# Kernel tuning notes

Measured on AMD Instinct MI355X. Metric: run time of the kernel, lower is better.

The kernel has to match this reference:

```python
import jax, jax.numpy as jnp
import numpy as np

DT = 0.5
T_STEPS = int(2500 / DT)   # 5000
T_STIM = int(2000 / DT)    # 4000
A = 270.0; B_ = 108.0; D_ = 0.154; GAMMA = 0.641; TAU_S = 100.0; TAU_AMPA = 2.0
BATCH = 4096


def setup_inputs() -> dict:
    key = jax.random.key(0)
    k0, k1, k2, k3, k4 = jax.random.split(key, 5)
    return {
        "input_signal": jax.random.normal(k0, (BATCH, 1), dtype=jnp.float32),
        "J11": jnp.float32(0.2609), "J12": jnp.float32(0.0497),
        "J21": jnp.float32(0.0497), "J22": jnp.float32(0.2609),
        "J_ext": jnp.float32(0.0156), "I_0": jnp.float32(0.3255),
        "noise_ampa": jnp.float32(0.02), "threshold": jnp.float32(0.5),
        "motor_delay": jnp.float32(0.1),
        "eps0_1": jax.random.normal(k1, (BATCH, 1), dtype=jnp.float32),
        "eps0_2": jax.random.normal(k2, (BATCH, 1), dtype=jnp.float32),
        "eps_1": jax.random.normal(k3, (T_STEPS, BATCH, 1), dtype=jnp.float32),
        "eps_2": jax.random.normal(k4, (T_STEPS, BATCH, 1), dtype=jnp.float32),
    }


def _H(x):
    # Wong-Wang f-I curve: relu((a x - b) / (1 - exp(-d (a x - b)) + 1e-6))
    u = A * x - B_
    return jax.nn.relu(u / (1.0 - jnp.exp(-D_ * u) + 1e-6))


def _simulate(input_signal, J11, J12, J21, J22, J_ext, I_0, noise_ampa,
              eps0_1, eps0_2, eps_1, eps_2):
    decay = jnp.exp(jnp.float32(-DT / TAU_AMPA))
    nscale = jnp.float32(np.sqrt((1.0 - np.exp(-2.0 * DT / TAU_AMPA)) / 2.0))
    s0 = jnp.full_like(input_signal, 0.1)  # [B,1]
    carry0 = (s0, s0, eps0_1 * noise_ampa, eps0_2 * noise_ampa)

    def step(carry, xs):
        s1, s2, In1, In2 = carry
        e1, e2, t = xs
        stim = t < T_STIM
        I1 = jnp.where(stim, J_ext * (1.0 + input_signal / 100.0), 0.0)
        I2 = jnp.where(stim, J_ext * (1.0 - input_signal / 100.0), 0.0)
        x1 = J11 * s1 - J12 * s2 + I_0 + I1 + In1
        x2 = J22 * s2 - J21 * s1 + I_0 + I2 + In2
        ds1 = -(s1 / TAU_S) + (1.0 - s1) * _H(x1) * GAMMA / 1000.0
        ds2 = -(s2 / TAU_S) + (1.0 - s2) * _H(x2) * GAMMA / 1000.0
        In1n = In1 * decay + noise_ampa * nscale * e1
        In2n = In2 * decay + noise_ampa * nscale * e2
        s1n = s1 + ds1 * DT
        s2n = s2 + ds2 * DT
        ys = (jnp.concatenate([s1n, s2n], axis=-1),   # trajectory row [B,2]
              jnp.concatenate([ds1, ds2], axis=-1))   # dsdt row [B,2]
        return (s1n, s2n, In1n, In2n), ys

    ts = jnp.arange(T_STEPS)
    _, (traj, dsdt) = jax.lax.scan(step, carry0, (eps_1, eps_2, ts))
    return traj, dsdt  # each [T, B, 2]


def _decide(traj_m):
    # traj_m = trajectory - threshold; first-crossing times per unit
    m1 = traj_m[:, :, 0] > 0
    m2 = traj_m[:, :, 1] > 0
    inf = jnp.float32(jnp.inf)
    t1 = jnp.where(m1.any(0), jnp.argmax(m1, axis=0).astype(jnp.float32), inf)
    t2 = jnp.where(m2.any(0), jnp.argmax(m2, axis=0).astype(jnp.float32), inf)
    dtimes = jnp.where(t1 < t2, t1, -t2)
    return dtimes * DT


def reference(input_signal, J11, J12, J21, J22, J_ext, I_0, noise_ampa,
              threshold, motor_delay, eps0_1, eps0_2, eps_1, eps_2):
    traj, dsdt = _simulate(input_signal, J11, J12, J21, J22, J_ext, I_0,
                           noise_ampa, eps0_1, eps0_2, eps_1, eps_2)
    out = _decide(traj - threshold)  # [B], signed decision time in ms
    out = jnp.where(out < 0, out / 1000.0 - motor_delay,
                    jnp.where(out > 0, out / 1000.0 + motor_delay, out))
    return out
```

## Files before the change

kernel.cpp:

```cpp
#include <hip/hip_runtime.h>

#define BATCHN 4096
#define NSTEPS 5000
#define NSTIM  4000
#define U      25
#define NBLK      (NSTEPS / U)
#define NBLK_STIM (NSTIM / U)
#define ELPB   32

static __device__ __forceinline__ float swap_pair(float v) {
    return __int_as_float(
        __builtin_amdgcn_mov_dpp(__float_as_int(v), 0xB1, 0xF, 0xF, true));
}

__global__ __launch_bounds__(128, 1) void ww_kernel(
    const float* __restrict__ input_signal,
    const float* __restrict__ sJ11, const float* __restrict__ sJ12,
    const float* __restrict__ sJ21, const float* __restrict__ sJ22,
    const float* __restrict__ sJext, const float* __restrict__ sI0,
    const float* __restrict__ sNoise, const float* __restrict__ sThr,
    const float* __restrict__ sDelay,
    const float* __restrict__ eps0_1, const float* __restrict__ eps0_2,
    const float* __restrict__ eps_1, const float* __restrict__ eps_2,
    float* __restrict__ out)
{
    __shared__ float slab[2][U][64];
    __shared__ float strc[2][U][64];
    __shared__ int done1;
    __shared__ int exit_blk;

    const int tid  = threadIdx.x;
    const int lane = tid & 63;
    const int wave = tid >> 6;
    const int unit = lane & 1;

    const float KE = -0.22217503629690245f;

    if (wave == 0) {
        __builtin_amdgcn_s_setprio(3);
        const float J11 = sJ11[0], J12 = sJ12[0], J21 = sJ21[0], J22 = sJ22[0];
        const float K270 = KE * 270.0f;
        const float B11 = K270 * J11, nB12 = -K270 * J12;
        const float B22 = K270 * J22, nB21 = -K270 * J21;
        const float Bs = unit ? B22 : B11;
        const float Bc = unit ? nB21 : nB12;
        const float nKE  = -KE;
        const float KE1p = 1.000001f * KE;
        const float SM = 0.995f;
        const float QC = 3.205e-4f;

        float s = 0.1f;

        if (lane == 0) { done1 = 0; exit_blk = 0x7fffffff; }
        __syncthreads();
        bool wrote = false;
        for (int blk = 0; blk < NBLK; ++blk) {
            if (blk >= *(volatile int*)&exit_blk) break;
            if (!wrote && *(volatile int*)&done1) {
                if (lane == 0) exit_blk = blk + 1;
                wrote = true;
            }
            const int sl = blk & 1;
            const float* __restrict__ base = &slab[sl][0][lane];
            float* __restrict__ trc = &strc[sl][0][lane];
            float k0 = base[0];
            float k1 = base[64];
            #pragma unroll
            for (int i = 0; i < U; ++i) {
                float kc = k0;
                k0 = k1;
                if (i + 2 < U) k1 = base[(i + 2) * 64];
                float sc = swap_pair(s);
                float w  = fmaf(Bs, s, fmaf(Bc, sc, kc));
                float x  = __builtin_amdgcn_exp2f(w);
                float r  = __builtin_amdgcn_rcpf(fmaf(nKE, x, KE1p));
                float h  = fmaxf(w * r, 0.0f);
                s = fmaf(h, fmaf(-QC, s, QC), SM * s);
                trc[i * 64] = s;
            }
            __syncthreads();
        }
        return;
    }

    const int b = blockIdx.x * ELPB + (lane >> 1);
    const float noise = sNoise[0];
    const float Jext = sJext[0], I0 = sI0[0];
    const float thr = sThr[0], delay = sDelay[0];

    const float inp = input_signal[b];
    const float Pself = unit
        ? fmaf(270.0f, I0 + Jext * (1.0f - inp * 0.01f), -108.0f)
        : fmaf(270.0f, I0 + Jext * (1.0f + inp * 0.01f), -108.0f);
    const float Pn  = fmaf(270.0f, I0, -108.0f);
    const float KPs = KE * Pself, KPn = KE * Pn;

    const float decay = 0.7788007830714049f;
    const float kKE   = KE * noise * 0.4435478165294536f * 270.0f;
    const float n270K = noise * 270.0f * KE;

    const float* __restrict__ ep = (unit ? eps_2 : eps_1) + b;
    float VK = (unit ? eps0_2[b] : eps0_1[b]) * n270K;

    auto fill = [&](int blk) {
        const int sl = blk & 1;
        const size_t off = (size_t)blk * U * BATCHN;
        const float KP = (blk < NBLK_STIM) ? KPs : KPn;
        float* __restrict__ dst = &slab[sl][0][lane];
        float r[U];
        #pragma unroll
        for (int i = 0; i < U; ++i)
            r[i] = ep[off + (size_t)i * BATCHN];
        #pragma unroll
        for (int i = 0; i < U; ++i) {
            dst[i * 64] = VK + KP;
            VK = fmaf(VK, decay, kKE * r[i]);
        }
    };

    const float INF = __builtin_inff();
    float tm = INF;
    float tf = 0.0f;
    bool mydone = false;

    auto scan = [&](int blk) {
        const int sl = blk & 1;
        const float* __restrict__ src = &strc[sl][0][lane];
        #pragma unroll
        for (int i = 0; i < U; ++i) {
            float sv = src[i * 64];
            tm = fminf(tm, (sv > thr) ? tf : INF);
            tf += 1.0f;
        }
    };

    fill(0);
    __syncthreads();
    for (int blk = 0; blk < NBLK; ++blk) {
        if (blk >= *(volatile int*)&exit_blk) break;
        if (blk + 1 < NBLK) fill(blk + 1);
        if (blk >= 1) {
            scan(blk - 1);
            if (!mydone) {
                float pm = fminf(tm, swap_pair(tm));
                if (__all(pm < INF)) {
                    if (lane == 0) done1 = 1;
                    mydone = true;
                }
            }
        }
        __syncthreads();
    }
    if (!mydone) scan(NBLK - 1);

    float to = swap_pair(tm);
    if (unit == 0) {
        float t1 = tm, t2 = to;
        float o;
        if (t1 == INF && t2 == INF) {
            o = -3.0e38f;
        } else {
            float dtm = (t1 < t2) ? t1 : -t2;
            o = dtm * 0.5f;
            if (o < 0.0f)      o = o / 1000.0f - delay;
            else if (o > 0.0f) o = o / 1000.0f + delay;
        }
        out[b] = o;
    }
}

extern "C" void kernel_launch(void* const* d_in, const int* in_sizes, int n_in,
                              void* d_out, int out_size, void* d_ws, size_t ws_size,
                              hipStream_t stream) {
    ww_kernel<<<dim3(BATCHN / ELPB), dim3(128), 0, stream>>>(
        (const float*)d_in[0],
        (const float*)d_in[1],
        (const float*)d_in[2],
        (const float*)d_in[3],
        (const float*)d_in[4],
        (const float*)d_in[5],
        (const float*)d_in[6],
        (const float*)d_in[7],
        (const float*)d_in[8],
        (const float*)d_in[9],
        (const float*)d_in[10],
        (const float*)d_in[11],
        (const float*)d_in[12],
        (const float*)d_in[13],
        (float*)d_out);
}
```

Measured before the change: 428.7 us.

## Merge producer and consumer waves into one wave with register double-buffered noise

Replaces the two-wave design, where a loader wave filled LDS slabs and a compute wave ran the recurrence, with a single wave per block. That wave prefetches noise into two register buffers, computes the noise recurrence inline, and checks the threshold crossing on the fly. This removes the LDS traffic, the barriers and the shared early-exit flags. The cost is that global load latency is no longer hidden by a separate wave and must be covered by software prefetch one block ahead, and register pressure goes up.

```diff
diff --git a/kernel.cpp b/kernel.cpp
--- a/kernel.cpp
+++ b/kernel.cpp
@@ -13,7 +13,7 @@
         __builtin_amdgcn_mov_dpp(__float_as_int(v), 0xB1, 0xF, 0xF, true));
 }
 
-__global__ __launch_bounds__(128, 1) void ww_kernel(
+__global__ __launch_bounds__(64, 1) void ww_kernel(
     const float* __restrict__ input_signal,
     const float* __restrict__ sJ11, const float* __restrict__ sJ12,
     const float* __restrict__ sJ21, const float* __restrict__ sJ22,
@@ -24,66 +24,23 @@
     const float* __restrict__ eps_1, const float* __restrict__ eps_2,
     float* __restrict__ out)
 {
-    __shared__ float slab[2][U][64];
-    __shared__ float strc[2][U][64];
-    __shared__ int done1;
-    __shared__ int exit_blk;
-
-    const int tid  = threadIdx.x;
-    const int lane = tid & 63;
-    const int wave = tid >> 6;
+    const int lane = threadIdx.x;
     const int unit = lane & 1;
+    const int b    = blockIdx.x * ELPB + (lane >> 1);
 
     const float KE = -0.22217503629690245f;
 
-    if (wave == 0) {
-        __builtin_amdgcn_s_setprio(3);
-        const float J11 = sJ11[0], J12 = sJ12[0], J21 = sJ21[0], J22 = sJ22[0];
-        const float K270 = KE * 270.0f;
-        const float B11 = K270 * J11, nB12 = -K270 * J12;
-        const float B22 = K270 * J22, nB21 = -K270 * J21;
-        const float Bs = unit ? B22 : B11;
-        const float Bc = unit ? nB21 : nB12;
-        const float nKE  = -KE;
-        const float KE1p = 1.000001f * KE;
-        const float SM = 0.995f;
-        const float QC = 3.205e-4f;
+    const float J11 = sJ11[0], J12 = sJ12[0], J21 = sJ21[0], J22 = sJ22[0];
+    const float K270 = KE * 270.0f;
+    const float B11 = K270 * J11, nB12 = -K270 * J12;
+    const float B22 = K270 * J22, nB21 = -K270 * J21;
+    const float Bs = unit ? B22 : B11;
+    const float Bc = unit ? nB21 : nB12;
+    const float nKE  = -KE;
+    const float KE1p = 1.000001f * KE;
+    const float SM = 0.995f;
+    const float QC = 3.205e-4f;
 
-        float s = 0.1f;
-
-        if (lane == 0) { done1 = 0; exit_blk = 0x7fffffff; }
-        __syncthreads();
-        bool wrote = false;
-        for (int blk = 0; blk < NBLK; ++blk) {
-            if (blk >= *(volatile int*)&exit_blk) break;
-            if (!wrote && *(volatile int*)&done1) {
-                if (lane == 0) exit_blk = blk + 1;
-                wrote = true;
-            }
-            const int sl = blk & 1;
-            const float* __restrict__ base = &slab[sl][0][lane];
-            float* __restrict__ trc = &strc[sl][0][lane];
-            float k0 = base[0];
-            float k1 = base[64];
-            #pragma unroll
-            for (int i = 0; i < U; ++i) {
-                float kc = k0;
-                k0 = k1;
-                if (i + 2 < U) k1 = base[(i + 2) * 64];
-                float sc = swap_pair(s);
-                float w  = fmaf(Bs, s, fmaf(Bc, sc, kc));
-                float x  = __builtin_amdgcn_exp2f(w);
-                float r  = __builtin_amdgcn_rcpf(fmaf(nKE, x, KE1p));
-                float h  = fmaxf(w * r, 0.0f);
-                s = fmaf(h, fmaf(-QC, s, QC), SM * s);
-                trc[i * 64] = s;
-            }
-            __syncthreads();
-        }
-        return;
-    }
-
-    const int b = blockIdx.x * ELPB + (lane >> 1);
     const float noise = sNoise[0];
     const float Jext = sJext[0], I0 = sI0[0];
     const float thr = sThr[0], delay = sDelay[0];
@@ -102,56 +59,46 @@
     const float* __restrict__ ep = (unit ? eps_2 : eps_1) + b;
     float VK = (unit ? eps0_2[b] : eps0_1[b]) * n270K;
 
-    auto fill = [&](int blk) {
-        const int sl = blk & 1;
-        const size_t off = (size_t)blk * U * BATCHN;
-        const float KP = (blk < NBLK_STIM) ? KPs : KPn;
-        float* __restrict__ dst = &slab[sl][0][lane];
-        float r[U];
-        #pragma unroll
-        for (int i = 0; i < U; ++i)
-            r[i] = ep[off + (size_t)i * BATCHN];
-        #pragma unroll
-        for (int i = 0; i < U; ++i) {
-            dst[i * 64] = VK + KP;
-            VK = fmaf(VK, decay, kKE * r[i]);
-        }
-    };
-
+    float s = 0.1f;
     const float INF = __builtin_inff();
     float tm = INF;
     float tf = 0.0f;
-    bool mydone = false;
 
-    auto scan = [&](int blk) {
-        const int sl = blk & 1;
-        const float* __restrict__ src = &strc[sl][0][lane];
+    float bufA[U], bufB[U];
+
+    auto loadE = [&](float (&buf)[U], int blk) {
+        const size_t off = (size_t)blk * ((size_t)U * BATCHN);
+        #pragma unroll
+        for (int i = 0; i < U; ++i)
+            buf[i] = ep[off + (size_t)i * BATCHN];
+    };
+
+    auto stepBlk = [&](const float (&buf)[U], int blk) -> bool {
+        const float KP = (blk < NBLK_STIM) ? KPs : KPn;
         #pragma unroll
         for (int i = 0; i < U; ++i) {
-            float sv = src[i * 64];
-            tm = fminf(tm, (sv > thr) ? tf : INF);
+            float kc = VK + KP;
+            VK = fmaf(VK, decay, kKE * buf[i]);
+            float sc = swap_pair(s);
+            float w  = fmaf(Bs, s, fmaf(Bc, sc, kc));
+            float x  = __builtin_amdgcn_exp2f(w);
+            float r  = __builtin_amdgcn_rcpf(fmaf(nKE, x, KE1p));
+            float h  = fmaxf(w * r, 0.0f);
+            s = fmaf(h, fmaf(-QC, s, QC), SM * s);
+            tm = fminf(tm, (s > thr) ? tf : INF);
             tf += 1.0f;
         }
+        float pm = fminf(tm, swap_pair(tm));
+        return __all(pm < INF);
     };
 
-    fill(0);
-    __syncthreads();
-    for (int blk = 0; blk < NBLK; ++blk) {
-        if (blk >= *(volatile int*)&exit_blk) break;
-        if (blk + 1 < NBLK) fill(blk + 1);
-        if (blk >= 1) {
-            scan(blk - 1);
-            if (!mydone) {
-                float pm = fminf(tm, swap_pair(tm));
-                if (__all(pm < INF)) {
-                    if (lane == 0) done1 = 1;
-                    mydone = true;
-                }
-            }
-        }
-        __syncthreads();
+    loadE(bufA, 0);
+    for (int blk = 0; blk < NBLK; blk += 2) {
+        loadE(bufB, blk + 1);
+        if (stepBlk(bufA, blk)) break;
+        if (blk + 2 < NBLK) loadE(bufA, blk + 2);
+        if (stepBlk(bufB, blk + 1)) break;
     }
-    if (!mydone) scan(NBLK - 1);
 
     float to = swap_pair(tm);
     if (unit == 0) {
@@ -172,7 +119,7 @@
 extern "C" void kernel_launch(void* const* d_in, const int* in_sizes, int n_in,
                               void* d_out, int out_size, void* d_ws, size_t ws_size,
                               hipStream_t stream) {
-    ww_kernel<<<dim3(BATCHN / ELPB), dim3(128), 0, stream>>>(
+    ww_kernel<<<dim3(BATCHN / ELPB), dim3(64), 0, stream>>>(
         (const float*)d_in[0],
         (const float*)d_in[1],
         (const float*)d_in[2],
```

New measurement: 421.5 us. About the same (-1.7%).
